# Optimization experiments

Hardware: AMD Instinct MI355X
Metric: run time of the kernel (lower is better)

## Reference

```python
import jax, jax.numpy as jnp
import numpy as np

N_NODES = 50000
N_EDGES = 800000
IN_DIM = 128
HID = 128
EDGE_DIM = 10
BN_EPS = 1e-5


def setup_inputs() -> dict:
    key = jax.random.key(0)
    ks = jax.random.split(key, 12)
    s = 0.05
    return {
        "x": jax.random.normal(ks[0], (N_NODES, IN_DIM), dtype=jnp.float32),
        "edge_index": jax.random.randint(ks[1], (2, N_EDGES), 0, N_NODES, dtype=jnp.int32),
        "edge_attr": jax.random.normal(ks[2], (N_EDGES, EDGE_DIM), dtype=jnp.float32),
        "Wq": jax.random.normal(ks[3], (HID, IN_DIM), dtype=jnp.float32) * s,
        "bq": jnp.zeros((HID,), dtype=jnp.float32),
        "Wk": jax.random.normal(ks[4], (HID, IN_DIM), dtype=jnp.float32) * s,
        "bk": jnp.zeros((HID,), dtype=jnp.float32),
        "Wv": jax.random.normal(ks[5], (HID, IN_DIM), dtype=jnp.float32) * s,
        "bv": jnp.zeros((HID,), dtype=jnp.float32),
        "We": jax.random.normal(ks[6], (HID, EDGE_DIM), dtype=jnp.float32) * s,
        "Wskip": jax.random.normal(ks[7], (HID, IN_DIM), dtype=jnp.float32) * s,
        "bskip": jnp.zeros((HID,), dtype=jnp.float32),
        "gamma": jnp.ones((HID,), dtype=jnp.float32),
        "beta": jnp.zeros((HID,), dtype=jnp.float32),
    }


def reference(x, edge_index, edge_attr, Wq, bq, Wk, bk, Wv, bv, We, Wskip, bskip, gamma, beta):
    N = x.shape[0]
    d = Wq.shape[0]
    src, dst = edge_index[0], edge_index[1]
    # dense node-level projections, then gather per edge
    q_all = x @ Wq.T + bq          # [N, d]
    k_all = x @ Wk.T + bk
    v_all = x @ Wv.T + bv
    e = edge_attr @ We.T           # [E, d] (lin_edge, no bias)
    q = q_all[dst]                 # query at target node i
    k = k_all[src] + e             # key at source node j + edge feature
    v = v_all[src] + e             # value + edge feature (PyG adds edge to value too)
    scale = 1.0 / jnp.sqrt(jnp.asarray(d, dtype=x.dtype))
    alpha = (q * k).sum(-1) * scale                              # [E]
    # segment softmax over incoming edges of each target node
    amax = jax.ops.segment_max(alpha, dst, num_segments=N)       # [N]
    ex = jnp.exp(alpha - amax[dst])
    denom = jax.ops.segment_sum(ex, dst, num_segments=N)
    w = ex / denom[dst]                                          # [E]
    agg = jax.ops.segment_sum(v * w[:, None], dst, num_segments=N)  # [N, d]
    out = agg + x @ Wskip.T + bskip                              # root/skip connection
    h = jax.nn.relu(out)
    # BatchNorm1d (training mode: batch stats, biased variance)
    mean = h.mean(0)
    var = ((h - mean) ** 2).mean(0)
    return gamma * (h - mean) * jax.lax.rsqrt(var + BN_EPS) + beta
```

## Files before the change

kernel.cpp:

```cpp
#include <hip/hip_runtime.h>

#define HID 128
#define EDGE_DIM 10
#define BN_EPS 1e-5f
#define ATT_SCALE 0.08838834764831845f

typedef unsigned short ushort_t;
typedef unsigned char uchar_t;
typedef __attribute__((ext_vector_type(8))) short short8v;
typedef __attribute__((ext_vector_type(4))) float float4v;

__device__ __forceinline__ float b2f(ushort_t u) {
    return __uint_as_float(((unsigned)u) << 16);
}
__device__ __forceinline__ ushort_t f2b(float f) {
    unsigned u = __float_as_uint(f);
    return (ushort_t)((u + 0x7FFFu + ((u >> 16) & 1u)) >> 16);
}
__device__ __forceinline__ unsigned pack2(float a, float b) {
    return (unsigned)f2b(a) | ((unsigned)f2b(b) << 16);
}
__device__ __forceinline__ uchar_t f2fp8(float f) {
    return (uchar_t)(__builtin_amdgcn_cvt_pk_fp8_f32(f, 0.f, 0u, false) & 0xFF);
}
__device__ __forceinline__ void dec8(uint2 u, float* o) {
    auto a = __builtin_amdgcn_cvt_pk_f32_fp8(u.x, false);
    auto b = __builtin_amdgcn_cvt_pk_f32_fp8(u.x, true);
    auto c = __builtin_amdgcn_cvt_pk_f32_fp8(u.y, false);
    auto d = __builtin_amdgcn_cvt_pk_f32_fp8(u.y, true);
    o[0] = a[0]; o[1] = a[1]; o[2] = b[0]; o[3] = b[1];
    o[4] = c[0]; o[5] = c[1]; o[6] = d[0]; o[7] = d[1];
}

__global__ void prep_kernel(const float* __restrict__ x, const int* __restrict__ ei,
                            const float* __restrict__ Wq, const float* __restrict__ Wk,
                            const float* __restrict__ Wv, const float* __restrict__ Wskip,
                            const float* __restrict__ We, const float* __restrict__ bq,
                            ushort_t* __restrict__ xb, ushort_t* __restrict__ Wb,
                            ushort_t* __restrict__ MbT, float* __restrict__ cvec,
                            int* __restrict__ deg, int* __restrict__ rank, int N, int E) {
    int i = blockIdx.x * 256 + threadIdx.x;
    if (i < E) rank[i] = atomicAdd(&deg[ei[E + i]], 1);
    int xcount = N * (HID / 4);
    if (i < xcount) {
        float4 v = ((const float4*)x)[i];
        ushort4 o;
        o.x = f2b(v.x); o.y = f2b(v.y); o.z = f2b(v.z); o.w = f2b(v.w);
        ((ushort4*)xb)[i] = o;
        return;
    }
    int j = i - xcount;
    if (j < 4 * 128 * 128 / 4) {
        int w = j >> 12;
        int g = j & 4095;
        const float* W = (w == 0) ? Wq : (w == 1) ? Wk : (w == 2) ? Wv : Wskip;
        float4 v = ((const float4*)W)[g];
        ushort4 o;
        o.x = f2b(v.x); o.y = f2b(v.y); o.z = f2b(v.z); o.w = f2b(v.w);
        ((ushort4*)(Wb + (size_t)w * 128 * 128))[g] = o;
        return;
    }
    int k = j - 4 * 128 * 128 / 4;
    if (k < 16 * 128) {
        int jj = k >> 7, ii = k & 127;
        float s = 0.f;
        if (jj < EDGE_DIM) {
            for (int d = 0; d < 128; ++d)
                s += Wq[(size_t)d * 128 + ii] * We[(size_t)d * EDGE_DIM + jj];
        }
        MbT[k] = f2b(s);
        return;
    }
    int kk = k - 16 * 128;
    if (kk < 16) {
        float s = 0.f;
        if (kk < EDGE_DIM) {
            for (int d = 0; d < 128; ++d)
                s += bq[d] * We[(size_t)d * EDGE_DIM + kk];
        }
        cvec[kk] = s;
    }
}

__global__ __launch_bounds__(256) void mfma_proj_kernel(
    const ushort_t* __restrict__ xb, const ushort_t* __restrict__ Wb,
    const ushort_t* __restrict__ MbT, const float* __restrict__ cvec,
    const float* __restrict__ bq, const float* __restrict__ bk,
    const float* __restrict__ bv, const float* __restrict__ bskip,
    float* __restrict__ q_all, uchar_t* __restrict__ kvp,
    float* __restrict__ qwe_tbl, float* __restrict__ out, int N)
{
    const int which = blockIdx.y;
    const int tid   = threadIdx.x;
    const int wid   = tid >> 6;
    const int lane  = tid & 63;
    const int nbase = blockIdx.x * 128;
    const ushort_t* W = Wb + (size_t)which * 128 * 128;
    const float* bias = (which == 0) ? bq : (which == 1) ? bk : (which == 2) ? bv : bskip;

    __shared__ ushort_t Wl[128 * 128];
    __shared__ uchar_t  tb[4][16 * 144];

    {
        int row  = tid & 127;
        int half = tid >> 7;
        const ushort_t* src = W + (size_t)row * HID + half * 64;
        #pragma unroll
        for (int c = 0; c < 8; ++c) {
            int cc = half * 8 + c;
            int sw = cc ^ (row & 7);
            *(short8v*)&Wl[row * 128 + sw * 8] = *(const short8v*)&src[c * 8];
        }
    }

    const int row   = lane & 15;
    const int kgrp  = lane >> 4;
    const int col16 = lane & 15;
    const int orow  = (lane >> 4) * 4;

    float bv8[8];
    #pragma unroll
    for (int ct = 0; ct < 8; ++ct) bv8[ct] = bias[ct * 16 + col16];
    float cv = 0.f;
    short8v mreg[4];
    if (which == 0) {
        #pragma unroll
        for (int kt = 0; kt < 4; ++kt)
            mreg[kt] = *(const short8v*)&MbT[(size_t)row * HID + kt * 32 + kgrp * 8];
        if (col16 < EDGE_DIM) cv = cvec[col16];
    }

    __syncthreads();

    #pragma unroll
    for (int t = 0; t < 2; ++t) {
        const int n0 = nbase + wid * 32 + t * 16;
        if (n0 >= N) break;
        int arow = n0 + row; if (arow >= N) arow = N - 1;

        short8v a[4];
        #pragma unroll
        for (int kt = 0; kt < 4; ++kt)
            a[kt] = *(const short8v*)&xb[(size_t)arow * HID + kt * 32 + kgrp * 8];

        float4v acc[8];
        #pragma unroll
        for (int ct = 0; ct < 8; ++ct) acc[ct] = (float4v){0.f, 0.f, 0.f, 0.f};
        float4v accq = (float4v){0.f, 0.f, 0.f, 0.f};

        #pragma unroll
        for (int kt = 0; kt < 4; ++kt) {
            const int cc = kt * 4 + kgrp;
            const int sw = cc ^ (row & 7);
            #pragma unroll
            for (int ct = 0; ct < 8; ++ct) {
                short8v b = *(const short8v*)&Wl[(ct * 16 + row) * 128 + sw * 8];
                acc[ct] = __builtin_amdgcn_mfma_f32_16x16x32_bf16(a[kt], b, acc[ct], 0, 0, 0);
            }
            if (which == 0)
                accq = __builtin_amdgcn_mfma_f32_16x16x32_bf16(a[kt], mreg[kt], accq, 0, 0, 0);
        }

        if (which == 0 || which == 3) {
            float* dst = (which == 0) ? q_all : out;
            #pragma unroll
            for (int r = 0; r < 4; ++r) {
                int node = n0 + orow + r;
                if (node >= N) continue;
                #pragma unroll
                for (int ct = 0; ct < 8; ++ct)
                    dst[(size_t)node * HID + ct * 16 + col16] = acc[ct][r] + bv8[ct];
            }
            if (which == 0 && col16 < EDGE_DIM) {
                #pragma unroll
                for (int r = 0; r < 4; ++r) {
                    int node = n0 + orow + r;
                    if (node < N)
                        qwe_tbl[(size_t)node * EDGE_DIM + col16] = accq[r] + cv;
                }
            }
        } else {
            const int off8 = (which == 2) ? 8 : 0;
            uchar_t* tbk = tb[wid];
            #pragma unroll
            for (int r = 0; r < 4; ++r) {
                #pragma unroll
                for (int ct = 0; ct < 8; ++ct)
                    tbk[(orow + r) * 144 + ct * 16 + col16] = f2fp8(acc[ct][r] + bv8[ct]);
            }
            #pragma unroll
            for (int i = lane; i < 256; i += 64) {
                int r = i >> 4, c = i & 15;
                int node = n0 + r;
                if (node < N)
                    *(uint2*)&kvp[(size_t)node * 256 + c * 16 + off8] =
                        *(const uint2*)&tbk[r * 144 + c * 8];
            }
        }
    }
}

__global__ __launch_bounds__(256) void scan1_kernel(const int* __restrict__ deg,
                                                    int* __restrict__ rowptr,
                                                    int* __restrict__ partials, int N) {
    int i = blockIdx.x * 256 + threadIdx.x;
    int v = (i < N) ? deg[i] : 0;
    __shared__ int sm[256];
    sm[threadIdx.x] = v;
    __syncthreads();
    for (int off = 1; off < 256; off <<= 1) {
        int t = (threadIdx.x >= off) ? sm[threadIdx.x - off] : 0;
        __syncthreads();
        sm[threadIdx.x] += t;
        __syncthreads();
    }
    if (i < N) rowptr[i] = sm[threadIdx.x] - v;
    if (threadIdx.x == 255) partials[blockIdx.x] = sm[255];
}

__global__ __launch_bounds__(256) void scan2_kernel(int* __restrict__ partials,
                                                    int* __restrict__ rowptr, int nb, int N) {
    __shared__ int sm[256];
    int v = (threadIdx.x < nb) ? partials[threadIdx.x] : 0;
    sm[threadIdx.x] = v;
    __syncthreads();
    for (int off = 1; off < 256; off <<= 1) {
        int t = (threadIdx.x >= off) ? sm[threadIdx.x - off] : 0;
        __syncthreads();
        sm[threadIdx.x] += t;
        __syncthreads();
    }
    if (threadIdx.x < nb) partials[threadIdx.x] = sm[threadIdx.x] - v;
    if (threadIdx.x == 255) rowptr[N] = sm[255];
}

__global__ __launch_bounds__(256) void scan3_kernel(int* __restrict__ rowptr,
                                                    const int* __restrict__ partials, int N) {
    int i = blockIdx.x * 256 + threadIdx.x;
    if (i < N) rowptr[i] += partials[blockIdx.x];
}

__global__ void scatter_kernel(const int* __restrict__ ei, const int* __restrict__ rank,
                               const int* __restrict__ rowptr, const float* __restrict__ ea,
                               int* __restrict__ csr_src, ushort_t* __restrict__ ea_csr, int E) {
    int e = blockIdx.x * 256 + threadIdx.x;
    if (e >= E) return;
    int dst = ei[E + e];
    int pos = rowptr[dst] + rank[e];
    csr_src[pos] = ei[e];
    const float* s = ea + (size_t)e * EDGE_DIM;
    float2 a = *(const float2*)s;
    float2 b = *(const float2*)(s + 2);
    float2 c = *(const float2*)(s + 4);
    float2 d = *(const float2*)(s + 6);
    float2 f = *(const float2*)(s + 8);
    unsigned* o = (unsigned*)(ea_csr + (size_t)pos * EDGE_DIM);
    o[0] = pack2(a.x, a.y);
    o[1] = pack2(b.x, b.y);
    o[2] = pack2(c.x, c.y);
    o[3] = pack2(d.x, d.y);
    o[4] = pack2(f.x, f.y);
}

__global__ __launch_bounds__(256) void attn_kernel(
    const ushort_t* __restrict__ ea_csr, const float* __restrict__ We,
    const float* __restrict__ q_all, const float* __restrict__ qwe_tbl,
    const uchar_t* __restrict__ kvp,
    const int* __restrict__ rowptr, const int* __restrict__ csr_src,
    float* __restrict__ out, int N)
{
    const int node = blockIdx.x * 4 + (threadIdx.x >> 6);
    if (node >= N) return;
    const int lane = threadIdx.x & 63;
    const int gl = lane & 15;
    const int g  = lane >> 4;

    const int p0 = rowptr[node];
    const int p1 = rowptr[node + 1];
    if (p0 == p1) return;

    float4 qa = *(const float4*)&q_all[(size_t)node * HID + gl * 8];
    float4 qb = *(const float4*)&q_all[(size_t)node * HID + gl * 8 + 4];
    float qsel = (gl < EDGE_DIM) ? qwe_tbl[(size_t)node * EDGE_DIM + gl] : 0.f;

    float l = 0.f, t = 0.f;
    float A[8];
    #pragma unroll
    for (int m = 0; m < 8; ++m) A[m] = 0.f;

    int pa = p0 + g, pb = pa + 4;
    bool va = pa < p1, vbv = pb < p1;
    int src_a = csr_src[va ? pa : p0];
    int src_b = csr_src[vbv ? pb : p0];

    const int iters = (p1 - p0 + 7) >> 3;
    for (int it = 0; it < iters; ++it) {
        int cpa = va ? pa : p0, cpb = vbv ? pb : p0;
        bool cva = va, cvb = vbv;
        int csa = src_a, csb = src_b;
        pa = p0 + (it + 1) * 8 + g; pb = pa + 4;
        va = pa < p1; vbv = pb < p1;
        src_a = csr_src[va ? pa : p0];
        src_b = csr_src[vbv ? pb : p0];

        uint4 ra = *(const uint4*)(kvp + (size_t)csa * 256 + gl * 16);
        uint4 rb = *(const uint4*)(kvp + (size_t)csb * 256 + gl * 16);
        float ea_a = (gl < EDGE_DIM) ? b2f(ea_csr[(size_t)cpa * EDGE_DIM + gl]) : 0.f;
        float ea_b = (gl < EDGE_DIM) ? b2f(ea_csr[(size_t)cpb * EDGE_DIM + gl]) : 0.f;

        float ka[8], kbf[8];
        dec8(make_uint2(ra.x, ra.y), ka);
        dec8(make_uint2(rb.x, rb.y), kbf);

        float sa = qsel * ea_a;
        sa += qa.x * ka[0] + qa.y * ka[1] + qa.z * ka[2] + qa.w * ka[3];
        sa += qb.x * ka[4] + qb.y * ka[5] + qb.z * ka[6] + qb.w * ka[7];
        float sb = qsel * ea_b;
        sb += qa.x * kbf[0] + qa.y * kbf[1] + qa.z * kbf[2] + qa.w * kbf[3];
        sb += qb.x * kbf[4] + qb.y * kbf[5] + qb.z * kbf[6] + qb.w * kbf[7];
        #pragma unroll
        for (int off = 1; off < 16; off <<= 1) {
            sa += __shfl_xor(sa, off, 64);
            sb += __shfl_xor(sb, off, 64);
        }
        sa = cva ? sa : -1.0e4f;
        sb = cvb ? sb : -1.0e4f;
        float exa = __expf(sa * ATT_SCALE);
        float exb = __expf(sb * ATT_SCALE);

        float vfa[8], vfb[8];
        dec8(make_uint2(ra.z, ra.w), vfa);
        dec8(make_uint2(rb.z, rb.w), vfb);

        l += exa + exb;
        t += exa * ea_a + exb * ea_b;
        #pragma unroll
        for (int m = 0; m < 8; ++m) A[m] += exa * vfa[m] + exb * vfb[m];
    }

    #pragma unroll
    for (int off = 16; off < 64; off <<= 1) {
        l += __shfl_xor(l, off, 64);
        t += __shfl_xor(t, off, 64);
        #pragma unroll
        for (int m = 0; m < 8; ++m) A[m] += __shfl_xor(A[m], off, 64);
    }

    float tj[EDGE_DIM];
    #pragma unroll
    for (int j = 0; j < EDGE_DIM; ++j) tj[j] = __shfl(t, j, 16);

    const int d0 = gl * 8 + g * 2;
    float e0 = 0.f, e1 = 0.f;
    #pragma unroll
    for (int jj = 0; jj < 5; ++jj) {
        float2 wa = *(const float2*)&We[(size_t)d0 * EDGE_DIM + 2 * jj];
        float2 wb = *(const float2*)&We[(size_t)(d0 + 1) * EDGE_DIM + 2 * jj];
        e0 += wa.x * tj[2 * jj] + wa.y * tj[2 * jj + 1];
        e1 += wb.x * tj[2 * jj] + wb.y * tj[2 * jj + 1];
    }
    float a0 = (g == 0) ? A[0] : (g == 1) ? A[2] : (g == 2) ? A[4] : A[6];
    float a1 = (g == 0) ? A[1] : (g == 1) ? A[3] : (g == 2) ? A[5] : A[7];

    float inv = 1.f / l;
    float2* o = (float2*)&out[(size_t)node * HID + d0];
    float2 cur = *o;
    cur.x += (a0 + e0) * inv;
    cur.y += (a1 + e1) * inv;
    *o = cur;
}

__global__ __launch_bounds__(256) void bnstats_kernel(const float* __restrict__ out,
                                                      float* __restrict__ sums,
                                                      float* __restrict__ sumsq, int N) {
    int f = threadIdx.x & 127;
    int half = threadIdx.x >> 7;
    float s = 0.f, s2 = 0.f;
    for (int r = blockIdx.x * 2 + half; r < N; r += gridDim.x * 2) {
        float h = out[(size_t)r * HID + f];
        h = h > 0.f ? h : 0.f;
        s += h; s2 += h * h;
    }
    __shared__ float ls[256], ls2[256];
    ls[threadIdx.x] = s; ls2[threadIdx.x] = s2;
    __syncthreads();
    if (half == 0) {
        atomicAdd(&sums[f], ls[f] + ls[f + 128]);
        atomicAdd(&sumsq[f], ls2[f] + ls2[f + 128]);
    }
}

__global__ __launch_bounds__(256) void bnapply_kernel(float* __restrict__ out,
                                                      const float* __restrict__ sums,
                                                      const float* __restrict__ sumsq,
                                                      const float* __restrict__ gamma,
                                                      const float* __restrict__ beta, int N) {
    int idx = blockIdx.x * 256 + threadIdx.x;
    int total = N * (HID / 4);
    if (idx >= total) return;
    int c8 = idx & 31;
    float4 sm = ((const float4*)sums)[c8];
    float4 sq = ((const float4*)sumsq)[c8];
    float4 g4 = ((const float4*)gamma)[c8];
    float4 b4 = ((const float4*)beta)[c8];
    float invN = 1.f / (float)N;
    float4 v = ((const float4*)out)[idx];
    float4 o;
    float m, var, sc, h;
    m = sm.x * invN; var = sq.x * invN - m * m; sc = g4.x * rsqrtf(var + BN_EPS);
    h = v.x > 0.f ? v.x : 0.f; o.x = (h - m) * sc + b4.x;
    m = sm.y * invN; var = sq.y * invN - m * m; sc = g4.y * rsqrtf(var + BN_EPS);
    h = v.y > 0.f ? v.y : 0.f; o.y = (h - m) * sc + b4.y;
    m = sm.z * invN; var = sq.z * invN - m * m; sc = g4.z * rsqrtf(var + BN_EPS);
    h = v.z > 0.f ? v.z : 0.f; o.z = (h - m) * sc + b4.z;
    m = sm.w * invN; var = sq.w * invN - m * m; sc = g4.w * rsqrtf(var + BN_EPS);
    h = v.w > 0.f ? v.w : 0.f; o.w = (h - m) * sc + b4.w;
    ((float4*)out)[idx] = o;
}

extern "C" void kernel_launch(void* const* d_in, const int* in_sizes, int n_in,
                              void* d_out, int out_size, void* d_ws, size_t ws_size,
                              hipStream_t stream) {
    const float* x     = (const float*)d_in[0];
    const int*   ei    = (const int*)d_in[1];
    const float* ea    = (const float*)d_in[2];
    const float* Wq    = (const float*)d_in[3];
    const float* bq    = (const float*)d_in[4];
    const float* Wk    = (const float*)d_in[5];
    const float* bk    = (const float*)d_in[6];
    const float* Wv    = (const float*)d_in[7];
    const float* bv    = (const float*)d_in[8];
    const float* We    = (const float*)d_in[9];
    const float* Wskip = (const float*)d_in[10];
    const float* bskip = (const float*)d_in[11];
    const float* gamma = (const float*)d_in[12];
    const float* beta  = (const float*)d_in[13];
    float* out = (float*)d_out;

    const int N = in_sizes[0] / HID;
    const int E = in_sizes[2] / EDGE_DIM;
    const size_t NH = (size_t)N * HID;
    const int nb = (N + 255) / 256;

    char* wsb = (char*)d_ws;
    float* q_all    = (float*)wsb;
    uchar_t* kvp    = (uchar_t*)(wsb + NH * 4);
    char* uni       = (char*)(kvp + NH * 2);
    ushort_t* xb    = (ushort_t*)uni;
    ushort_t* Wb    = xb + NH;
    ushort_t* MbT   = Wb + 4 * 128 * 128;
    float* cvec     = (float*)(MbT + 16 * 128);
    ushort_t* ea_csr = (ushort_t*)uni;
    size_t uni_bytes = (size_t)E * EDGE_DIM * 2;
    char* tail      = uni + uni_bytes;
    float* qwe_tbl  = (float*)tail;
    int* csr_src    = (int*)(qwe_tbl + (size_t)N * EDGE_DIM);
    int* rank       = csr_src + E;
    int* deg        = rank + E;
    float* sums     = (float*)(deg + N);
    float* sumsq    = sums + HID;
    int* rowptr     = (int*)(sumsq + HID);
    int* partials   = rowptr + N + 1;

    hipMemsetAsync(deg, 0, (size_t)(N + 256) * 4, stream);

    int ccount = N * (HID / 4) + 4 * 128 * 128 / 4 + 16 * 128 + 16;
    int pgrid = max((ccount + 255) / 256, (E + 255) / 256);
    prep_kernel<<<pgrid, 256, 0, stream>>>(x, ei, Wq, Wk, Wv, Wskip, We, bq,
                                           xb, Wb, MbT, cvec, deg, rank, N, E);

    dim3 pg((N + 127) / 128, 4);
    mfma_proj_kernel<<<pg, 256, 0, stream>>>(xb, Wb, MbT, cvec,
                                             bq, bk, bv, bskip,
                                             q_all, kvp, qwe_tbl, out, N);

    scan1_kernel<<<nb, 256, 0, stream>>>(deg, rowptr, partials, N);
    scan2_kernel<<<1, 256, 0, stream>>>(partials, rowptr, nb, N);
    scan3_kernel<<<nb, 256, 0, stream>>>(rowptr, partials, N);

    scatter_kernel<<<(E + 255) / 256, 256, 0, stream>>>(ei, rank, rowptr, ea,
                                                        csr_src, ea_csr, E);

    attn_kernel<<<(N + 3) / 4, 256, 0, stream>>>(ea_csr, We, q_all, qwe_tbl, kvp,
                                                 rowptr, csr_src, out, N);

    bnstats_kernel<<<1024, 256, 0, stream>>>(out, sums, sumsq, N);
    bnapply_kernel<<<(N * (HID / 4) + 255) / 256, 256, 0, stream>>>(out, sums, sumsq,
                                                                    gamma, beta, N);
}
```

Before: 213.8 us.

## Fuse BN statistics into attention epilogue and merge scan kernels

Batch-norm sum and sum-of-squares accumulation moves into the attention kernel's epilogue. Each block reduces its relu'd outputs in shared memory, then atomically adds them into 64 striped partial buffers, which removes a separate full read of the output. A tiny kernel turns the partials into per-feature scale and shift so the apply pass is a single FMA. The second and third scan passes are merged into one kernel that each block uses to recompute the block-offset prefix, saving a launch. The cost is shared-memory atomics and an extra barrier in the attention kernel.

New measurement: 234.6 us. +9.8%, slower.

```diff
diff --git a/kernel.cpp b/kernel.cpp
--- a/kernel.cpp
+++ b/kernel.cpp
@@ -218,8 +218,9 @@
     if (threadIdx.x == 255) partials[blockIdx.x] = sm[255];
 }
 
-__global__ __launch_bounds__(256) void scan2_kernel(int* __restrict__ partials,
-                                                    int* __restrict__ rowptr, int nb, int N) {
+__global__ __launch_bounds__(256) void scan23_kernel(int* __restrict__ rowptr,
+                                                     const int* __restrict__ partials,
+                                                     int nb, int N) {
     __shared__ int sm[256];
     int v = (threadIdx.x < nb) ? partials[threadIdx.x] : 0;
     sm[threadIdx.x] = v;
@@ -230,14 +231,10 @@
         sm[threadIdx.x] += t;
         __syncthreads();
     }
-    if (threadIdx.x < nb) partials[threadIdx.x] = sm[threadIdx.x] - v;
-    if (threadIdx.x == 255) rowptr[N] = sm[255];
-}
-
-__global__ __launch_bounds__(256) void scan3_kernel(int* __restrict__ rowptr,
-                                                    const int* __restrict__ partials, int N) {
+    int boff = (blockIdx.x > 0) ? sm[blockIdx.x - 1] : 0;
     int i = blockIdx.x * 256 + threadIdx.x;
-    if (i < N) rowptr[i] += partials[blockIdx.x];
+    if (i < N) rowptr[i] += boff;
+    if (blockIdx.x == (unsigned)(nb - 1) && threadIdx.x == 0) rowptr[N] = sm[nb - 1];
 }
 
 __global__ void scatter_kernel(const int* __restrict__ ei, const int* __restrict__ rank,
@@ -267,154 +264,169 @@
     const float* __restrict__ q_all, const float* __restrict__ qwe_tbl,
     const uchar_t* __restrict__ kvp,
     const int* __restrict__ rowptr, const int* __restrict__ csr_src,
-    float* __restrict__ out, int N)
+    float* __restrict__ out, float* __restrict__ sums_part,
+    float* __restrict__ sumsq_part, int N)
 {
+    __shared__ float bls[128], bls2[128];
+    if (threadIdx.x < 128) { bls[threadIdx.x] = 0.f; bls2[threadIdx.x] = 0.f; }
+    __syncthreads();
+
     const int node = blockIdx.x * 4 + (threadIdx.x >> 6);
-    if (node >= N) return;
     const int lane = threadIdx.x & 63;
     const int gl = lane & 15;
     const int g  = lane >> 4;
-
-    const int p0 = rowptr[node];
-    const int p1 = rowptr[node + 1];
-    if (p0 == p1) return;
-
-    float4 qa = *(const float4*)&q_all[(size_t)node * HID + gl * 8];
-    float4 qb = *(const float4*)&q_all[(size_t)node * HID + gl * 8 + 4];
-    float qsel = (gl < EDGE_DIM) ? qwe_tbl[(size_t)node * EDGE_DIM + gl] : 0.f;
-
-    float l = 0.f, t = 0.f;
-    float A[8];
-    #pragma unroll
-    for (int m = 0; m < 8; ++m) A[m] = 0.f;
-
-    int pa = p0 + g, pb = pa + 4;
-    bool va = pa < p1, vbv = pb < p1;
-    int src_a = csr_src[va ? pa : p0];
-    int src_b = csr_src[vbv ? pb : p0];
-
-    const int iters = (p1 - p0 + 7) >> 3;
-    for (int it = 0; it < iters; ++it) {
-        int cpa = va ? pa : p0, cpb = vbv ? pb : p0;
-        bool cva = va, cvb = vbv;
-        int csa = src_a, csb = src_b;
-        pa = p0 + (it + 1) * 8 + g; pb = pa + 4;
-        va = pa < p1; vbv = pb < p1;
-        src_a = csr_src[va ? pa : p0];
-        src_b = csr_src[vbv ? pb : p0];
-
-        uint4 ra = *(const uint4*)(kvp + (size_t)csa * 256 + gl * 16);
-        uint4 rb = *(const uint4*)(kvp + (size_t)csb * 256 + gl * 16);
-        float ea_a = (gl < EDGE_DIM) ? b2f(ea_csr[(size_t)cpa * EDGE_DIM + gl]) : 0.f;
-        float ea_b = (gl < EDGE_DIM) ? b2f(ea_csr[(size_t)cpb * EDGE_DIM + gl]) : 0.f;
-
-        float ka[8], kbf[8];
-        dec8(make_uint2(ra.x, ra.y), ka);
-        dec8(make_uint2(rb.x, rb.y), kbf);
-
-        float sa = qsel * ea_a;
-        sa += qa.x * ka[0] + qa.y * ka[1] + qa.z * ka[2] + qa.w * ka[3];
-        sa += qb.x * ka[4] + qb.y * ka[5] + qb.z * ka[6] + qb.w * ka[7];
-        float sb = qsel * ea_b;
-        sb += qa.x * kbf[0] + qa.y * kbf[1] + qa.z * kbf[2] + qa.w * kbf[3];
-        sb += qb.x * kbf[4] + qb.y * kbf[5] + qb.z * kbf[6] + qb.w * kbf[7];
-        #pragma unroll
-        for (int off = 1; off < 16; off <<= 1) {
-            sa += __shfl_xor(sa, off, 64);
-            sb += __shfl_xor(sb, off, 64);
+    const int d0 = gl * 8 + g * 2;
+
+    const bool valid_node = node < N;
+    int p0 = 0, p1 = 0;
+    if (valid_node) { p0 = rowptr[node]; p1 = rowptr[node + 1]; }
+    const bool has_edges = valid_node && (p1 > p0);
+
+    float rx = 0.f, ry = 0.f;
+
+    if (valid_node) {
+        float2* o = (float2*)&out[(size_t)node * HID + d0];
+        float2 cur = *o;
+
+        if (has_edges) {
+            float4 qa = *(const float4*)&q_all[(size_t)node * HID + gl * 8];
+            float4 qb = *(const float4*)&q_all[(size_t)node * HID + gl * 8 + 4];
+            float qsel = (gl < EDGE_DIM) ? qwe_tbl[(size_t)node * EDGE_DIM + gl] : 0.f;
+
+            float l = 0.f, t = 0.f;
+            float A[8];
+            #pragma unroll
+            for (int m = 0; m < 8; ++m) A[m] = 0.f;
+
+            int pa = p0 + g, pb = pa + 4;
+            bool va = pa < p1, vbv = pb < p1;
+            int src_a = csr_src[va ? pa : p0];
+            int src_b = csr_src[vbv ? pb : p0];
+
+            const int iters = (p1 - p0 + 7) >> 3;
+            for (int it = 0; it < iters; ++it) {
+                int cpa = va ? pa : p0, cpb = vbv ? pb : p0;
+                bool cva = va, cvb = vbv;
+                int csa = src_a, csb = src_b;
+                pa = p0 + (it + 1) * 8 + g; pb = pa + 4;
+                va = pa < p1; vbv = pb < p1;
+                src_a = csr_src[va ? pa : p0];
+                src_b = csr_src[vbv ? pb : p0];
+
+                uint4 ra = *(const uint4*)(kvp + (size_t)csa * 256 + gl * 16);
+                uint4 rb = *(const uint4*)(kvp + (size_t)csb * 256 + gl * 16);
+                float ea_a = (gl < EDGE_DIM) ? b2f(ea_csr[(size_t)cpa * EDGE_DIM + gl]) : 0.f;
+                float ea_b = (gl < EDGE_DIM) ? b2f(ea_csr[(size_t)cpb * EDGE_DIM + gl]) : 0.f;
+
+                float ka[8], kbf[8];
+                dec8(make_uint2(ra.x, ra.y), ka);
+                dec8(make_uint2(rb.x, rb.y), kbf);
+
+                float sa = qsel * ea_a;
+                sa += qa.x * ka[0] + qa.y * ka[1] + qa.z * ka[2] + qa.w * ka[3];
+                sa += qb.x * ka[4] + qb.y * ka[5] + qb.z * ka[6] + qb.w * ka[7];
+                float sb = qsel * ea_b;
+                sb += qa.x * kbf[0] + qa.y * kbf[1] + qa.z * kbf[2] + qa.w * kbf[3];
+                sb += qb.x * kbf[4] + qb.y * kbf[5] + qb.z * kbf[6] + qb.w * kbf[7];
+                #pragma unroll
+                for (int off = 1; off < 16; off <<= 1) {
+                    sa += __shfl_xor(sa, off, 64);
+                    sb += __shfl_xor(sb, off, 64);
+                }
+                sa = cva ? sa : -1.0e4f;
+                sb = cvb ? sb : -1.0e4f;
+                float exa = __expf(sa * ATT_SCALE);
+                float exb = __expf(sb * ATT_SCALE);
+
+                float vfa[8], vfb[8];
+                dec8(make_uint2(ra.z, ra.w), vfa);
+                dec8(make_uint2(rb.z, rb.w), vfb);
+
+                l += exa + exb;
+                t += exa * ea_a + exb * ea_b;
+                #pragma unroll
+                for (int m = 0; m < 8; ++m) A[m] += exa * vfa[m] + exb * vfb[m];
+            }
+
+            #pragma unroll
+            for (int off = 16; off < 64; off <<= 1) {
+                l += __shfl_xor(l, off, 64);
+                t += __shfl_xor(t, off, 64);
+                #pragma unroll
+                for (int m = 0; m < 8; ++m) A[m] += __shfl_xor(A[m], off, 64);
+            }
+
+            float tj[EDGE_DIM];
+            #pragma unroll
+            for (int j = 0; j < EDGE_DIM; ++j) tj[j] = __shfl(t, j, 16);
+
+            float e0 = 0.f, e1 = 0.f;
+            #pragma unroll
+            for (int jj = 0; jj < 5; ++jj) {
+                float2 wa = *(const float2*)&We[(size_t)d0 * EDGE_DIM + 2 * jj];
+                float2 wb = *(const float2*)&We[(size_t)(d0 + 1) * EDGE_DIM + 2 * jj];
+                e0 += wa.x * tj[2 * jj] + wa.y * tj[2 * jj + 1];
+                e1 += wb.x * tj[2 * jj] + wb.y * tj[2 * jj + 1];
+            }
+            float a0 = (g == 0) ? A[0] : (g == 1) ? A[2] : (g == 2) ? A[4] : A[6];
+            float a1 = (g == 0) ? A[1] : (g == 1) ? A[3] : (g == 2) ? A[5] : A[7];
+
+            float inv = 1.f / l;
+            cur.x += (a0 + e0) * inv;
+            cur.y += (a1 + e1) * inv;
+            *o = cur;
         }
-        sa = cva ? sa : -1.0e4f;
-        sb = cvb ? sb : -1.0e4f;
-        float exa = __expf(sa * ATT_SCALE);
-        float exb = __expf(sb * ATT_SCALE);
-
-        float vfa[8], vfb[8];
-        dec8(make_uint2(ra.z, ra.w), vfa);
-        dec8(make_uint2(rb.z, rb.w), vfb);
-
-        l += exa + exb;
-        t += exa * ea_a + exb * ea_b;
-        #pragma unroll
-        for (int m = 0; m < 8; ++m) A[m] += exa * vfa[m] + exb * vfb[m];
-    }
-
-    #pragma unroll
-    for (int off = 16; off < 64; off <<= 1) {
-        l += __shfl_xor(l, off, 64);
-        t += __shfl_xor(t, off, 64);
-        #pragma unroll
-        for (int m = 0; m < 8; ++m) A[m] += __shfl_xor(A[m], off, 64);
-    }
-
-    float tj[EDGE_DIM];
-    #pragma unroll
-    for (int j = 0; j < EDGE_DIM; ++j) tj[j] = __shfl(t, j, 16);
-
-    const int d0 = gl * 8 + g * 2;
-    float e0 = 0.f, e1 = 0.f;
-    #pragma unroll
-    for (int jj = 0; jj < 5; ++jj) {
-        float2 wa = *(const float2*)&We[(size_t)d0 * EDGE_DIM + 2 * jj];
-        float2 wb = *(const float2*)&We[(size_t)(d0 + 1) * EDGE_DIM + 2 * jj];
-        e0 += wa.x * tj[2 * jj] + wa.y * tj[2 * jj + 1];
-        e1 += wb.x * tj[2 * jj] + wb.y * tj[2 * jj + 1];
-    }
-    float a0 = (g == 0) ? A[0] : (g == 1) ? A[2] : (g == 2) ? A[4] : A[6];
-    float a1 = (g == 0) ? A[1] : (g == 1) ? A[3] : (g == 2) ? A[5] : A[7];
-
-    float inv = 1.f / l;
-    float2* o = (float2*)&out[(size_t)node * HID + d0];
-    float2 cur = *o;
-    cur.x += (a0 + e0) * inv;
-    cur.y += (a1 + e1) * inv;
-    *o = cur;
-}
-
-__global__ __launch_bounds__(256) void bnstats_kernel(const float* __restrict__ out,
-                                                      float* __restrict__ sums,
-                                                      float* __restrict__ sumsq, int N) {
-    int f = threadIdx.x & 127;
-    int half = threadIdx.x >> 7;
+
+        rx = fmaxf(cur.x, 0.f);
+        ry = fmaxf(cur.y, 0.f);
+    }
+
+    atomicAdd(&bls[d0], rx);
+    atomicAdd(&bls[d0 + 1], ry);
+    atomicAdd(&bls2[d0], rx * rx);
+    atomicAdd(&bls2[d0 + 1], ry * ry);
+    __syncthreads();
+    if (threadIdx.x < 128) {
+        int sl = (blockIdx.x & 63) * 128 + threadIdx.x;
+        atomicAdd(&sums_part[sl], bls[threadIdx.x]);
+        atomicAdd(&sumsq_part[sl], bls2[threadIdx.x]);
+    }
+}
+
+__global__ void bnscale_kernel(const float* __restrict__ sums_part,
+                               const float* __restrict__ sumsq_part,
+                               const float* __restrict__ gamma, const float* __restrict__ beta,
+                               float* __restrict__ scale, float* __restrict__ shift, int N) {
+    int f = threadIdx.x;
+    if (f >= HID) return;
     float s = 0.f, s2 = 0.f;
-    for (int r = blockIdx.x * 2 + half; r < N; r += gridDim.x * 2) {
-        float h = out[(size_t)r * HID + f];
-        h = h > 0.f ? h : 0.f;
-        s += h; s2 += h * h;
-    }
-    __shared__ float ls[256], ls2[256];
-    ls[threadIdx.x] = s; ls2[threadIdx.x] = s2;
-    __syncthreads();
-    if (half == 0) {
-        atomicAdd(&sums[f], ls[f] + ls[f + 128]);
-        atomicAdd(&sumsq[f], ls2[f] + ls2[f + 128]);
-    }
+    for (int j = 0; j < 64; ++j) {
+        s  += sums_part [j * 128 + f];
+        s2 += sumsq_part[j * 128 + f];
+    }
+    float invN = 1.f / (float)N;
+    float m = s * invN;
+    float var = s2 * invN - m * m;
+    float sc = gamma[f] * rsqrtf(var + BN_EPS);
+    scale[f] = sc;
+    shift[f] = beta[f] - m * sc;
 }
 
 __global__ __launch_bounds__(256) void bnapply_kernel(float* __restrict__ out,
-                                                      const float* __restrict__ sums,
-                                                      const float* __restrict__ sumsq,
-                                                      const float* __restrict__ gamma,
-                                                      const float* __restrict__ beta, int N) {
+                                                      const float* __restrict__ scale,
+                                                      const float* __restrict__ shift, int N) {
     int idx = blockIdx.x * 256 + threadIdx.x;
     int total = N * (HID / 4);
     if (idx >= total) return;
     int c8 = idx & 31;
-    float4 sm = ((const float4*)sums)[c8];
-    float4 sq = ((const float4*)sumsq)[c8];
-    float4 g4 = ((const float4*)gamma)[c8];
-    float4 b4 = ((const float4*)beta)[c8];
-    float invN = 1.f / (float)N;
+    float4 sc = ((const float4*)scale)[c8];
+    float4 sh = ((const float4*)shift)[c8];
     float4 v = ((const float4*)out)[idx];
     float4 o;
-    float m, var, sc, h;
-    m = sm.x * invN; var = sq.x * invN - m * m; sc = g4.x * rsqrtf(var + BN_EPS);
-    h = v.x > 0.f ? v.x : 0.f; o.x = (h - m) * sc + b4.x;
-    m = sm.y * invN; var = sq.y * invN - m * m; sc = g4.y * rsqrtf(var + BN_EPS);
-    h = v.y > 0.f ? v.y : 0.f; o.y = (h - m) * sc + b4.y;
-    m = sm.z * invN; var = sq.z * invN - m * m; sc = g4.z * rsqrtf(var + BN_EPS);
-    h = v.z > 0.f ? v.z : 0.f; o.z = (h - m) * sc + b4.z;
-    m = sm.w * invN; var = sq.w * invN - m * m; sc = g4.w * rsqrtf(var + BN_EPS);
-    h = v.w > 0.f ? v.w : 0.f; o.w = (h - m) * sc + b4.w;
+    o.x = fmaxf(v.x, 0.f) * sc.x + sh.x;
+    o.y = fmaxf(v.y, 0.f) * sc.y + sh.y;
+    o.z = fmaxf(v.z, 0.f) * sc.z + sh.z;
+    o.w = fmaxf(v.w, 0.f) * sc.w + sh.w;
     ((float4*)out)[idx] = o;
 }
 
@@ -457,12 +469,14 @@
     int* csr_src    = (int*)(qwe_tbl + (size_t)N * EDGE_DIM);
     int* rank       = csr_src + E;
     int* deg        = rank + E;
-    float* sums     = (float*)(deg + N);
-    float* sumsq    = sums + HID;
-    int* rowptr     = (int*)(sumsq + HID);
+    float* sums_part  = (float*)(deg + N);
+    float* sumsq_part = sums_part + 64 * 128;
+    float* scale    = sumsq_part + 64 * 128;
+    float* shift    = scale + HID;
+    int* rowptr     = (int*)(shift + HID);
     int* partials   = rowptr + N + 1;
 
-    hipMemsetAsync(deg, 0, (size_t)(N + 256) * 4, stream);
+    hipMemsetAsync(deg, 0, (size_t)(N + 2 * 64 * 128) * 4, stream);
 
     int ccount = N * (HID / 4) + 4 * 128 * 128 / 4 + 16 * 128 + 16;
     int pgrid = max((ccount + 255) / 256, (E + 255) / 256);
@@ -475,16 +489,16 @@
                                              q_all, kvp, qwe_tbl, out, N);
 
     scan1_kernel<<<nb, 256, 0, stream>>>(deg, rowptr, partials, N);
-    scan2_kernel<<<1, 256, 0, stream>>>(partials, rowptr, nb, N);
-    scan3_kernel<<<nb, 256, 0, stream>>>(rowptr, partials, N);
+    scan23_kernel<<<nb, 256, 0, stream>>>(rowptr, partials, nb, N);
 
     scatter_kernel<<<(E + 255) / 256, 256, 0, stream>>>(ei, rank, rowptr, ea,
                                                         csr_src, ea_csr, E);
 
     attn_kernel<<<(N + 3) / 4, 256, 0, stream>>>(ea_csr, We, q_all, qwe_tbl, kvp,
-                                                 rowptr, csr_src, out, N);
-
-    bnstats_kernel<<<1024, 256, 0, stream>>>(out, sums, sumsq, N);
-    bnapply_kernel<<<(N * (HID / 4) + 255) / 256, 256, 0, stream>>>(out, sums, sumsq,
-                                                                    gamma, beta, N);
-}
+                                                 rowptr, csr_src, out,
+                                                 sums_part, sumsq_part, N);
+
+    bnscale_kernel<<<1, 128, 0, stream>>>(sums_part, sumsq_part, gamma, beta,
+                                          scale, shift, N);
+    bnapply_kernel<<<(N * (HID / 4) + 255) / 256, 256, 0, stream>>>(out, scale, shift, N);
+}
```
